# Performance work log

Measured on AMD Instinct MI355X. Metric: run time of the kernel, lower is better.

## Reference

```python
import jax, jax.numpy as jnp
import numpy as np

LEN = 128
HIDDEN = 64
B, N = 256, 2048
LN_EPS = 1e-3  # keras LayerNormalization default epsilon
NEG_FILL = -1.0e9


def setup_inputs() -> dict:
    key = jax.random.key(0)
    k_in, k_m, k_w1, k_w2 = jax.random.split(key, 4)
    inputs = jax.random.normal(k_in, (B, N, LEN), dtype=jnp.float32)
    mask = jax.random.randint(k_m, (B, N), 0, 2) > 0
    # He-normal init for Dense kernels, zeros for biases (keras defaults)
    W1 = jax.random.normal(k_w1, (LEN, HIDDEN), dtype=jnp.float32) * np.sqrt(2.0 / LEN)
    b1 = jnp.zeros((HIDDEN,), dtype=jnp.float32)
    W2 = jax.random.normal(k_w2, (HIDDEN, LEN), dtype=jnp.float32) * np.sqrt(2.0 / HIDDEN)
    b2 = jnp.zeros((LEN,), dtype=jnp.float32)
    gamma = jnp.ones((LEN,), dtype=jnp.float32)
    beta = jnp.zeros((LEN,), dtype=jnp.float32)
    return {"inputs": inputs, "mask": mask, "W1": W1, "b1": b1,
            "W2": W2, "b2": b2, "gamma": gamma, "beta": beta}


def reference(inputs, mask, W1, b1, W2, b2, gamma, beta):
    # MLP: Dense -> Dense -> LayerNorm -> ReLU (weights shared over nodes)
    h = jnp.einsum('bnd,dh->bnh', inputs, W1) + b1          # [B,N,HIDDEN]
    h = jnp.einsum('bnh,hd->bnd', h, W2) + b2               # [B,N,LEN]
    mu = jnp.mean(h, axis=-1, keepdims=True)
    var = jnp.mean(jnp.square(h - mu), axis=-1, keepdims=True)
    h = (h - mu) * jax.lax.rsqrt(var + LN_EPS) * gamma + beta
    x = jax.nn.relu(h)                                      # [B,N,LEN]
    # masked fill (masked-out nodes set to large negative before max-pool)
    x = jnp.where(mask[:, :, None], x, NEG_FILL)
    # global max-pool over all N nodes, broadcast back, concat local+global
    x_pool = jnp.max(x, axis=1, keepdims=True)              # [B,1,LEN]
    x_tile = jnp.broadcast_to(x_pool, x.shape)              # [B,N,LEN]
    return jnp.concatenate([x, x_tile], axis=-1)            # [B,N,2*LEN]
```

## Files before the change

### kernel.cpp

```cpp
#include <hip/hip_runtime.h>

#define NEG_FILL -1.0e9f

using bf16x8 = __attribute__((ext_vector_type(8))) short;
using s16x4  = __attribute__((ext_vector_type(4))) short;
using f32x4  = __attribute__((ext_vector_type(4))) float;

static __device__ __forceinline__ short f2bf(float f) {
    union { float f; unsigned u; } a; a.f = f;
    unsigned r = a.u + 0x7FFFu + ((a.u >> 16) & 1u);
    return (short)(r >> 16);
}


__global__ __launch_bounds__(256) void k_prep(
    const float* __restrict__ W1, const float* __restrict__ b1,
    const float* __restrict__ W2, const float* __restrict__ b2,
    short* __restrict__ WT, float* __restrict__ beff, int* __restrict__ pool)
{
    int blk = blockIdx.x, tid = threadIdx.x;
    if (blk < 128) {
        pool[blk * 256 + tid] = __float_as_int(NEG_FILL);
        return;
    }
    if (blk < 192) {
        int e = (blk - 128) * 256 + tid;
        int n = e >> 7, k = e & 127;
        float s = 0.f;
        #pragma unroll 8
        for (int h = 0; h < 64; ++h) s = fmaf(W1[k * 64 + h], W2[h * 128 + n], s);
        WT[e] = f2bf(s);
    } else if (tid < 128) {
        float s = b2[tid];
        for (int h = 0; h < 64; ++h) s = fmaf(b1[h], W2[h * 128 + tid], s);
        beff[tid] = s;
    }
}

__global__ __launch_bounds__(256) void k_main(
    const float* __restrict__ X, const int* __restrict__ mask,
    const short* __restrict__ WT, const float* __restrict__ beff,
    const float* __restrict__ gamma, const float* __restrict__ beta,
    float* __restrict__ out, int* __restrict__ pool)
{
    __shared__ short As[64][136];
    __shared__ short Ws[128][136];
    __shared__ int pool_s[128];

    const int tid = threadIdx.x;
    const int rowbase = blockIdx.x * 64;

    if (tid < 128) pool_s[tid] = __float_as_int(NEG_FILL);

    #pragma unroll
    for (int i = 0; i < 8; ++i) {
        int g = tid + i * 256;
        int n = g >> 4, koff = (g & 15) * 8;
        *(bf16x8*)&Ws[n][koff] = *(const bf16x8*)(WT + g * 8);
    }
    #pragma unroll
    for (int i = 0; i < 8; ++i) {
        int f = tid + i * 256;
        int r = f >> 5, c4 = (f & 31) * 4;
        float4 xv = *(const float4*)(X + (size_t)(rowbase + r) * 128 + c4);
        s16x4 sv;
        sv[0] = f2bf(xv.x); sv[1] = f2bf(xv.y); sv[2] = f2bf(xv.z); sv[3] = f2bf(xv.w);
        *(s16x4*)&As[r][c4] = sv;
    }
    __syncthreads();

    const int wave = tid >> 6, lane = tid & 63;
    const int c = lane & 15, q = lane >> 4;

    f32x4 acc[8];
    const f32x4 zero = {0.f, 0.f, 0.f, 0.f};
    #pragma unroll
    for (int t = 0; t < 8; ++t) acc[t] = zero;

    const int arow = wave * 16 + c;
    #pragma unroll
    for (int kk = 0; kk < 4; ++kk) {
        bf16x8 a = *(const bf16x8*)&As[arow][kk * 32 + q * 8];
        #pragma unroll
        for (int t = 0; t < 8; ++t) {
            bf16x8 b = *(const bf16x8*)&Ws[t * 16 + c][kk * 32 + q * 8];
            acc[t] = __builtin_amdgcn_mfma_f32_16x16x32_bf16(a, b, acc[t], 0, 0, 0);
        }
    }

    float be[8], ga[8], bt[8];
    #pragma unroll
    for (int t = 0; t < 8; ++t) {
        int n = t * 16 + c;
        be[t] = beff[n]; ga[t] = gamma[n]; bt[t] = beta[n];
    }

    float v[8][4];
    #pragma unroll
    for (int t = 0; t < 8; ++t)
        #pragma unroll
        for (int r = 0; r < 4; ++r) v[t][r] = acc[t][r] + be[t];

    #pragma unroll
    for (int r = 0; r < 4; ++r) {
        float s = 0.f, s2 = 0.f;
        #pragma unroll
        for (int t = 0; t < 8; ++t) { s += v[t][r]; s2 = fmaf(v[t][r], v[t][r], s2); }
        #pragma unroll
        for (int m = 1; m < 16; m <<= 1) {
            s  += __shfl_xor(s,  m, 64);
            s2 += __shfl_xor(s2, m, 64);
        }
        float mu  = s * (1.f / 128.f);
        float var = s2 * (1.f / 128.f) - mu * mu;
        float rs  = rsqrtf(var + 1e-3f);
        int rg = rowbase + wave * 16 + q * 4 + r;
        int mk = mask[rg];
        #pragma unroll
        for (int t = 0; t < 8; ++t) {
            float y = fmaf((v[t][r] - mu) * rs, ga[t], bt[t]);
            y = fmaxf(y, 0.f);
            y = mk ? y : NEG_FILL;
            v[t][r] = y;
            out[(size_t)rg * 256 + t * 16 + c] = y;
        }
    }

    #pragma unroll
    for (int t = 0; t < 8; ++t) {
        float pm = fmaxf(fmaxf(v[t][0], v[t][1]), fmaxf(v[t][2], v[t][3]));
        pm = fmaxf(pm, __shfl_xor(pm, 16, 64));
        pm = fmaxf(pm, __shfl_xor(pm, 32, 64));
        if (q == 0) atomicMax(&pool_s[t * 16 + c], __float_as_int(pm));
    }
    __syncthreads();
    if (tid < 128) {
        int b = rowbase >> 11;
        atomicMax(&pool[b * 128 + tid], pool_s[tid]);
    }
}

__global__ __launch_bounds__(256) void k_bcast(
    const float4* __restrict__ pool4, float4* __restrict__ out4)
{
    unsigned idx = blockIdx.x * 256 + threadIdx.x;
    unsigned row = idx >> 5;
    unsigned c4  = idx & 31;
    unsigned b   = row >> 11;
    out4[(size_t)row * 64 + 32 + c4] = pool4[b * 32 + c4];
}

extern "C" void kernel_launch(void* const* d_in, const int* in_sizes, int n_in,
                              void* d_out, int out_size, void* d_ws, size_t ws_size,
                              hipStream_t stream)
{
    const float* X     = (const float*)d_in[0];
    const int*   mask  = (const int*)d_in[1];
    const float* W1    = (const float*)d_in[2];
    const float* b1    = (const float*)d_in[3];
    const float* W2    = (const float*)d_in[4];
    const float* b2    = (const float*)d_in[5];
    const float* gamma = (const float*)d_in[6];
    const float* beta  = (const float*)d_in[7];
    float* out = (float*)d_out;

    short* WT   = (short*)d_ws;
    float* beff = (float*)((char*)d_ws + 32768);
    int*   pool = (int*)((char*)d_ws + 33280);

    k_prep<<<193, 256, 0, stream>>>(W1, b1, W2, b2, WT, beff, pool);
    k_main<<<8192, 256, 0, stream>>>(X, mask, WT, beff, gamma, beta, out, pool);
    k_bcast<<<65536, 256, 0, stream>>>((const float4*)pool, (float4*)out);
}
```

Before: 727.1 us.

## Load X directly into MFMA fragments and batch broadcast stores with nontemporal writes

The main kernel no longer stages X through a shared-memory A tile. Each lane reads its fragment straight from global memory as two float4 loads and packs it to bf16 with the HIP bf16 conversion intrinsics, which removes the LDS round trip and shrinks shared-memory use. The broadcast kernel now runs 16x fewer blocks, with each thread doing 16 stores, and uses nontemporal stores for the tiled pool half of the output. The global loads are strided by row (16 lanes reading different rows), which may coalesce worse than the previous row-contiguous staging loads.

Result: no change. 723.6 us (-0.5%).

```diff
diff --git a/kernel.cpp b/kernel.cpp
--- a/kernel.cpp
+++ b/kernel.cpp
@@ -1,15 +1,24 @@
 #include <hip/hip_runtime.h>
+#include <hip/hip_bf16.h>
 
 #define NEG_FILL -1.0e9f
 
 using bf16x8 = __attribute__((ext_vector_type(8))) short;
-using s16x4  = __attribute__((ext_vector_type(4))) short;
 using f32x4  = __attribute__((ext_vector_type(4))) float;
 
 static __device__ __forceinline__ short f2bf(float f) {
     union { float f; unsigned u; } a; a.f = f;
     unsigned r = a.u + 0x7FFFu + ((a.u >> 16) & 1u);
     return (short)(r >> 16);
+}
+
+static __device__ __forceinline__ bf16x8 pack8(float4 a, float4 b) {
+    union { __hip_bfloat162 h[4]; bf16x8 v; } u;
+    u.h[0] = __float22bfloat162_rn({a.x, a.y});
+    u.h[1] = __float22bfloat162_rn({a.z, a.w});
+    u.h[2] = __float22bfloat162_rn({b.x, b.y});
+    u.h[3] = __float22bfloat162_rn({b.z, b.w});
+    return u.v;
 }
 
 
@@ -43,7 +52,6 @@
     const float* __restrict__ gamma, const float* __restrict__ beta,
     float* __restrict__ out, int* __restrict__ pool)
 {
-    __shared__ short As[64][136];
     __shared__ short Ws[128][136];
     __shared__ int pool_s[128];
 
@@ -58,41 +66,36 @@
         int n = g >> 4, koff = (g & 15) * 8;
         *(bf16x8*)&Ws[n][koff] = *(const bf16x8*)(WT + g * 8);
     }
-    #pragma unroll
-    for (int i = 0; i < 8; ++i) {
-        int f = tid + i * 256;
-        int r = f >> 5, c4 = (f & 31) * 4;
-        float4 xv = *(const float4*)(X + (size_t)(rowbase + r) * 128 + c4);
-        s16x4 sv;
-        sv[0] = f2bf(xv.x); sv[1] = f2bf(xv.y); sv[2] = f2bf(xv.z); sv[3] = f2bf(xv.w);
-        *(s16x4*)&As[r][c4] = sv;
-    }
-    __syncthreads();
 
     const int wave = tid >> 6, lane = tid & 63;
     const int c = lane & 15, q = lane >> 4;
+    const int rowloc = wave * 16 + c;
+    const float* __restrict__ xrow = X + (size_t)(rowbase + rowloc) * 128;
+
+    float be[8], ga[8], bt[8];
+    #pragma unroll
+    for (int t = 0; t < 8; ++t) {
+        int n = t * 16 + c;
+        be[t] = beff[n]; ga[t] = gamma[n]; bt[t] = beta[n];
+    }
+
+    __syncthreads();
 
     f32x4 acc[8];
     const f32x4 zero = {0.f, 0.f, 0.f, 0.f};
     #pragma unroll
     for (int t = 0; t < 8; ++t) acc[t] = zero;
 
-    const int arow = wave * 16 + c;
     #pragma unroll
     for (int kk = 0; kk < 4; ++kk) {
-        bf16x8 a = *(const bf16x8*)&As[arow][kk * 32 + q * 8];
+        float4 x0 = *(const float4*)(xrow + kk * 32 + q * 8);
+        float4 x1 = *(const float4*)(xrow + kk * 32 + q * 8 + 4);
+        bf16x8 a = pack8(x0, x1);
         #pragma unroll
         for (int t = 0; t < 8; ++t) {
             bf16x8 b = *(const bf16x8*)&Ws[t * 16 + c][kk * 32 + q * 8];
             acc[t] = __builtin_amdgcn_mfma_f32_16x16x32_bf16(a, b, acc[t], 0, 0, 0);
         }
-    }
-
-    float be[8], ga[8], bt[8];
-    #pragma unroll
-    for (int t = 0; t < 8; ++t) {
-        int n = t * 16 + c;
-        be[t] = beff[n]; ga[t] = gamma[n]; bt[t] = beta[n];
     }
 
     float v[8][4];
@@ -141,13 +144,18 @@
 }
 
 __global__ __launch_bounds__(256) void k_bcast(
-    const float4* __restrict__ pool4, float4* __restrict__ out4)
+    const f32x4* __restrict__ pool4, f32x4* __restrict__ out4)
 {
-    unsigned idx = blockIdx.x * 256 + threadIdx.x;
-    unsigned row = idx >> 5;
-    unsigned c4  = idx & 31;
-    unsigned b   = row >> 11;
-    out4[(size_t)row * 64 + 32 + c4] = pool4[b * 32 + c4];
+    unsigned base = blockIdx.x * 256 + threadIdx.x;
+    #pragma unroll
+    for (int i = 0; i < 16; ++i) {
+        unsigned idx = base + (unsigned)i * (4096u * 256u);
+        unsigned row = idx >> 5;
+        unsigned c4  = idx & 31;
+        unsigned b   = row >> 11;
+        f32x4 pv = pool4[b * 32 + c4];
+        __builtin_nontemporal_store(pv, &out4[(size_t)row * 64 + 32 + c4]);
+    }
 }
 
 extern "C" void kernel_launch(void* const* d_in, const int* in_sizes, int n_in,
@@ -170,5 +178,5 @@
 
     k_prep<<<193, 256, 0, stream>>>(W1, b1, W2, b2, WT, beff, pool);
     k_main<<<8192, 256, 0, stream>>>(X, mask, WT, beff, gamma, beta, out, pool);
-    k_bcast<<<65536, 256, 0, stream>>>((const float4*)pool, (float4*)out);
+    k_bcast<<<4096, 256, 0, stream>>>((const f32x4*)pool, (f32x4*)out);
 }
```
